# Kernel tuning notes

Hardware: AMD Instinct MI355X
Metric: run time of the kernel (lower is better)

## Reference

```python
import jax, jax.numpy as jnp
import numpy as np

N_NODES = 100000
N_EDGES = 3200000
D_IN = 128
D_OUT = 128
LN_EPS = 1e-5


def setup_inputs() -> dict:
    key = jax.random.key(0)
    k1, k2, k3, k4 = jax.random.split(key, 4)
    x = jax.random.normal(k1, (N_NODES, D_IN), dtype=jnp.float32)
    edge_index = jax.random.randint(k2, (2, N_EDGES), 0, N_NODES, dtype=jnp.int64)
    edge_weight = jax.random.uniform(k3, (N_EDGES,), dtype=jnp.float32)
    W = jax.random.normal(k4, (D_IN, D_OUT), dtype=jnp.float32) * (1.0 / np.sqrt(D_IN))
    b = jnp.zeros((D_OUT,), dtype=jnp.float32)
    gamma = jnp.ones((D_OUT,), dtype=jnp.float32)
    beta = jnp.zeros((D_OUT,), dtype=jnp.float32)
    return {"x": x, "edge_index": edge_index, "edge_weight": edge_weight,
            "W": W, "b": b, "gamma": gamma, "beta": beta}


def _gcn_layer(x, edge_index, edge_weight, W, b, gamma, beta):
    n = x.shape[0]
    row, col = edge_index[0], edge_index[1]  # source -> target
    # add self-loops with weight 1 (PyG GCNConv default)
    loop = jnp.arange(n, dtype=edge_index.dtype)
    row_f = jnp.concatenate([row, loop])
    col_f = jnp.concatenate([col, loop])
    w_f = jnp.concatenate([edge_weight, jnp.ones((n,), dtype=edge_weight.dtype)])
    # symmetric normalization: deg^-1/2[row] * w * deg^-1/2[col]
    deg = jax.ops.segment_sum(w_f, col_f, num_segments=n)
    dis = jnp.where(deg > 0, jax.lax.rsqrt(jnp.maximum(deg, 1e-30)), 0.0)
    norm = dis[row_f] * w_f * dis[col_f]  # [E+N]
    # linear transform first (cheaper), then gather/scatter-add over edges
    h = x @ W  # [N, D_OUT]
    msgs = norm[:, None] * h[row_f]  # [E+N, D_OUT]
    agg = jax.ops.segment_sum(msgs, col_f, num_segments=n) + b
    # LayerNorm over features
    mu = jnp.mean(agg, axis=-1, keepdims=True)
    var = jnp.mean(jnp.square(agg - mu), axis=-1, keepdims=True)
    normed = (agg - mu) * jax.lax.rsqrt(var + LN_EPS) * gamma + beta
    # ReLU; dropout is identity in eval mode
    return jax.nn.relu(normed)


def reference(x, edge_index, edge_weight, W, b, gamma, beta):
    return _gcn_layer(x, edge_index, edge_weight, W, b, gamma, beta)
```

## Files before the change

kernel.cpp:

```cpp
#include <hip/hip_runtime.h>

#define LN_EPS 1e-5f
#define FIX_SCALE 33554432.0f
#define FIX_INV   (1.0f / 33554432.0f)
#define MASK40    ((1ULL << 40) - 1)

__device__ __forceinline__ unsigned pack_bf16x2(float lo, float hi) {
    unsigned a = __float_as_uint(lo), b = __float_as_uint(hi);
    a = (a + 0x7FFFu + ((a >> 16) & 1u)) >> 16;
    b = (b + 0x7FFFu + ((b >> 16) & 1u)) >> 16;
    return a | (b << 16);
}

__device__ __forceinline__ float2 unpack_bf16x2(unsigned u) {
    return make_float2(__uint_as_float(u << 16), __uint_as_float(u & 0xFFFF0000u));
}


__global__ __launch_bounds__(256) void init_packed(unsigned long long* __restrict__ packed, int n) {
    int i = blockIdx.x * 256 + threadIdx.x;
    if (i < n) packed[i] = (1ULL << 25);
}


__global__ __launch_bounds__(256) void gemm_hist(const float* __restrict__ x,
                                                 const float* __restrict__ W,
                                                 unsigned* __restrict__ hb, int n,
                                                 const int* __restrict__ ei,
                                                 const float* __restrict__ ew,
                                                 unsigned long long* __restrict__ packed,
                                                 unsigned short* __restrict__ rank,
                                                 int E, int histBlocks) {
    __shared__ float xt[128][64];
    __shared__ float Ws[128][64];
    const int tid = threadIdx.x;

    if ((int)blockIdx.x < histBlocks) {
        int e = blockIdx.x * 256 + tid;
        if (e < E) {
            int c = ei[(long long)E + e];
            unsigned long long inc = (1ULL << 40) | (unsigned long long)(ew[e] * FIX_SCALE + 0.5f);
            unsigned long long old = atomicAdd(&packed[c], inc);
            rank[e] = (unsigned short)(old >> 40);
        }
        return;
    }

    const int g = (int)blockIdx.x - histBlocks;
    const int brow = (g >> 1) * 64;
    const int chalf = g & 1;

    for (int i = tid; i < 64 * 32; i += 256) {
        int r = i >> 5, c4 = i & 31, k0 = c4 * 4;
        int gr = brow + r;
        float4 v = make_float4(0.f, 0.f, 0.f, 0.f);
        if (gr < n) v = *(const float4*)(x + (size_t)gr * 128 + k0);
        xt[k0 + 0][r] = v.x; xt[k0 + 1][r] = v.y;
        xt[k0 + 2][r] = v.z; xt[k0 + 3][r] = v.w;
    }
    for (int i = tid; i < 128 * 16; i += 256) {
        int k = i >> 4, c4 = i & 15;
        float4 v = *(const float4*)(W + (size_t)k * 128 + chalf * 64 + c4 * 4);
        *(float4*)&Ws[k][c4 * 4] = v;
    }
    __syncthreads();

    const int r0 = (tid >> 4) * 4;
    const int c0 = (tid & 15) * 4;
    float4 acc0 = make_float4(0, 0, 0, 0), acc1 = acc0, acc2 = acc0, acc3 = acc0;
    #pragma unroll 8
    for (int k = 0; k < 128; k++) {
        float4 xa = *(const float4*)&xt[k][r0];
        float4 wb = *(const float4*)&Ws[k][c0];
        acc0.x += xa.x * wb.x; acc0.y += xa.x * wb.y; acc0.z += xa.x * wb.z; acc0.w += xa.x * wb.w;
        acc1.x += xa.y * wb.x; acc1.y += xa.y * wb.y; acc1.z += xa.y * wb.z; acc1.w += xa.y * wb.w;
        acc2.x += xa.z * wb.x; acc2.y += xa.z * wb.y; acc2.z += xa.z * wb.z; acc2.w += xa.z * wb.w;
        acc3.x += xa.w * wb.x; acc3.y += xa.w * wb.y; acc3.z += xa.w * wb.z; acc3.w += xa.w * wb.w;
    }
    float4 accs[4] = {acc0, acc1, acc2, acc3};
    #pragma unroll
    for (int i = 0; i < 4; i++) {
        int gr = brow + r0 + i;
        if (gr < n) {
            uint2 p;
            p.x = pack_bf16x2(accs[i].x, accs[i].y);
            p.y = pack_bf16x2(accs[i].z, accs[i].w);
            *(uint2*)(hb + (size_t)gr * 64 + (chalf * 64 + c0) / 2) = p;
        }
    }
}

__global__ __launch_bounds__(256) void hist_edges_plain(const int* __restrict__ ei,
                                                        const float* __restrict__ w,
                                                        unsigned long long* __restrict__ packed, int E) {
    int e = blockIdx.x * 256 + threadIdx.x;
    if (e >= E) return;
    int c = ei[(long long)E + e];
    unsigned long long inc = (1ULL << 40) | (unsigned long long)(w[e] * FIX_SCALE + 0.5f);
    atomicAdd(&packed[c], inc);
}

__global__ __launch_bounds__(256) void gemm_xw(const float* __restrict__ x,
                                               const float* __restrict__ W,
                                               unsigned* __restrict__ hb, int n) {
    __shared__ float xt[128][64];
    __shared__ float Ws[128][64];
    const int tid = threadIdx.x;
    const int brow = blockIdx.x * 64;
    const int chalf = blockIdx.y;

    for (int i = tid; i < 64 * 32; i += 256) {
        int r = i >> 5, c4 = i & 31, k0 = c4 * 4;
        int gr = brow + r;
        float4 v = make_float4(0.f, 0.f, 0.f, 0.f);
        if (gr < n) v = *(const float4*)(x + (size_t)gr * 128 + k0);
        xt[k0 + 0][r] = v.x; xt[k0 + 1][r] = v.y;
        xt[k0 + 2][r] = v.z; xt[k0 + 3][r] = v.w;
    }
    for (int i = tid; i < 128 * 16; i += 256) {
        int k = i >> 4, c4 = i & 15;
        float4 v = *(const float4*)(W + (size_t)k * 128 + chalf * 64 + c4 * 4);
        *(float4*)&Ws[k][c4 * 4] = v;
    }
    __syncthreads();

    const int r0 = (tid >> 4) * 4;
    const int c0 = (tid & 15) * 4;
    float4 acc0 = make_float4(0, 0, 0, 0), acc1 = acc0, acc2 = acc0, acc3 = acc0;
    #pragma unroll 8
    for (int k = 0; k < 128; k++) {
        float4 xa = *(const float4*)&xt[k][r0];
        float4 wb = *(const float4*)&Ws[k][c0];
        acc0.x += xa.x * wb.x; acc0.y += xa.x * wb.y; acc0.z += xa.x * wb.z; acc0.w += xa.x * wb.w;
        acc1.x += xa.y * wb.x; acc1.y += xa.y * wb.y; acc1.z += xa.y * wb.z; acc1.w += xa.y * wb.w;
        acc2.x += xa.z * wb.x; acc2.y += xa.z * wb.y; acc2.z += xa.z * wb.z; acc2.w += xa.z * wb.w;
        acc3.x += xa.w * wb.x; acc3.y += xa.w * wb.y; acc3.z += xa.w * wb.z; acc3.w += xa.w * wb.w;
    }
    float4 accs[4] = {acc0, acc1, acc2, acc3};
    #pragma unroll
    for (int i = 0; i < 4; i++) {
        int gr = brow + r0 + i;
        if (gr < n) {
            uint2 p;
            p.x = pack_bf16x2(accs[i].x, accs[i].y);
            p.y = pack_bf16x2(accs[i].z, accs[i].w);
            *(uint2*)(hb + (size_t)gr * 64 + (chalf * 64 + c0) / 2) = p;
        }
    }
}


__global__ __launch_bounds__(256) void scan_bsums_dis(const unsigned long long* __restrict__ packed,
                                                      int* __restrict__ bsum,
                                                      float* __restrict__ dis, int n) {
    int base = blockIdx.x * 1024;
    int t = threadIdx.x;
    int s = 0;
    #pragma unroll
    for (int k = 0; k < 4; k++) {
        int i = base + t * 4 + k;
        if (i < n) {
            unsigned long long p = packed[i];
            s += (int)(p >> 40);
            float d = (float)(p & MASK40) * FIX_INV;
            dis[i] = rsqrtf(fmaxf(d, 1e-30f));
        }
    }
    #pragma unroll
    for (int off = 32; off; off >>= 1) s += __shfl_xor(s, off);
    __shared__ int wsum[4];
    if ((t & 63) == 0) wsum[t >> 6] = s;
    __syncthreads();
    if (t == 0) bsum[blockIdx.x] = wsum[0] + wsum[1] + wsum[2] + wsum[3];
}

__global__ __launch_bounds__(256) void scan_boff(const int* __restrict__ bsum,
                                                 int* __restrict__ boff, int B,
                                                 int* __restrict__ rp, int n, int E) {
    int t = threadIdx.x;
    int v[4]; int loc = 0;
    #pragma unroll
    for (int k = 0; k < 4; k++) {
        int i = t * 4 + k;
        v[k] = (i < B) ? bsum[i] : 0;
        loc += v[k];
    }
    int lane = t & 63, wv = t >> 6;
    int incl = loc;
    #pragma unroll
    for (int off = 1; off < 64; off <<= 1) {
        int tt = __shfl_up(incl, off);
        if (lane >= off) incl += tt;
    }
    __shared__ int wsum[4];
    if (lane == 63) wsum[wv] = incl;
    __syncthreads();
    int woff = 0;
    for (int k = 0; k < wv; k++) woff += wsum[k];
    int run = woff + incl - loc;
    #pragma unroll
    for (int k = 0; k < 4; k++) {
        int i = t * 4 + k;
        if (i < B) boff[i] = run;
        run += v[k];
    }
    if (t == 0) rp[n] = E;
}

__global__ __launch_bounds__(256) void scan_write(const unsigned long long* __restrict__ packed,
                                                  const int* __restrict__ boff,
                                                  int* __restrict__ rp, int n) {
    int base = blockIdx.x * 1024;
    int t = threadIdx.x;
    int v[4]; int loc = 0;
    #pragma unroll
    for (int k = 0; k < 4; k++) {
        int i = base + t * 4 + k;
        v[k] = (i < n) ? (int)(packed[i] >> 40) : 0;
        loc += v[k];
    }
    int lane = t & 63, wv = t >> 6;
    int incl = loc;
    #pragma unroll
    for (int off = 1; off < 64; off <<= 1) {
        int tt = __shfl_up(incl, off);
        if (lane >= off) incl += tt;
    }
    __shared__ int wsum[4];
    if (lane == 63) wsum[wv] = incl;
    __syncthreads();
    int woff = 0;
    for (int k = 0; k < wv; k++) woff += wsum[k];
    int run = boff[blockIdx.x] + woff + incl - loc;
    #pragma unroll
    for (int k = 0; k < 4; k++) {
        int i = base + t * 4 + k;
        if (i < n) { rp[i] = run; run += v[k]; }
    }
}


__global__ __launch_bounds__(256) void sort_edges_rank(const int* __restrict__ ei,
                                                       const float* __restrict__ w,
                                                       const float* __restrict__ dis,
                                                       const int* __restrict__ rp,
                                                       const unsigned short* __restrict__ rank,
                                                       int2* __restrict__ es, int E) {
    int e = blockIdx.x * 256 + threadIdx.x;
    if (e >= E) return;
    int r = ei[e], c = ei[(long long)E + e];
    int pos = rp[c] + (int)rank[e];
    es[pos] = make_int2(r, __float_as_int(dis[r] * w[e]));
}

__global__ __launch_bounds__(256) void sort_edges_cursor(const int* __restrict__ ei,
                                                         const float* __restrict__ w,
                                                         const float* __restrict__ dis,
                                                         const int* __restrict__ rp,
                                                         int* __restrict__ cursor,
                                                         int2* __restrict__ es, int E) {
    int e = blockIdx.x * 256 + threadIdx.x;
    if (e >= E) return;
    int r = ei[e], c = ei[(long long)E + e];
    int pos = rp[c] + atomicAdd(&cursor[c], 1);
    es[pos] = make_int2(r, __float_as_int(dis[r] * w[e]));
}


__global__ __launch_bounds__(256) void agg_ln(const int* __restrict__ rp,
                                              const int2* __restrict__ es,
                                              const unsigned* __restrict__ hb,
                                              const float* __restrict__ dis,
                                              const float* __restrict__ b,
                                              const float* __restrict__ gamma,
                                              const float* __restrict__ beta,
                                              float* __restrict__ out, int n) {
    const int wave = threadIdx.x >> 6;
    const int lane = threadIdx.x & 63;
    const int node = blockIdx.x * 4 + wave;
    if (node >= n) return;

    const int j0 = rp[node], j1 = rp[node + 1];
    const float ds = dis[node];

    float2 hs = unpack_bf16x2(hb[(size_t)node * 64 + lane]);
    float ax = ds * hs.x, ay = ds * hs.y;

    int j = j0;
    for (; j + 7 < j1; j += 8) {
        int2 ee[8]; unsigned uu[8];
        #pragma unroll
        for (int k = 0; k < 8; k++) ee[k] = es[j + k];
        #pragma unroll
        for (int k = 0; k < 8; k++) uu[k] = hb[(size_t)ee[k].x * 64 + lane];
        #pragma unroll
        for (int k = 0; k < 8; k++) {
            float c = __int_as_float(ee[k].y);
            float2 v = unpack_bf16x2(uu[k]);
            ax += c * v.x;
            ay += c * v.y;
        }
    }
    for (; j < j1; ++j) {
        int2 e0 = es[j];
        float2 v = unpack_bf16x2(hb[(size_t)e0.x * 64 + lane]);
        float c = __int_as_float(e0.y);
        ax += c * v.x;
        ay += c * v.y;
    }

    float2 bb = ((const float2*)b)[lane];
    float vx = ds * ax + bb.x;
    float vy = ds * ay + bb.y;

    float s = vx + vy;
    #pragma unroll
    for (int off = 32; off; off >>= 1) s += __shfl_xor(s, off);
    float mu = s * (1.0f / 128.0f);
    float dx = vx - mu, dy = vy - mu;
    float q = dx * dx + dy * dy;
    #pragma unroll
    for (int off = 32; off; off >>= 1) q += __shfl_xor(q, off);
    float rs = rsqrtf(q * (1.0f / 128.0f) + LN_EPS);

    float2 g = ((const float2*)gamma)[lane], be = ((const float2*)beta)[lane];
    float2 o;
    o.x = fmaxf(dx * rs * g.x + be.x, 0.f);
    o.y = fmaxf(dy * rs * g.y + be.y, 0.f);
    ((float2*)(out + (size_t)node * 128))[lane] = o;
}


extern "C" void kernel_launch(void* const* d_in, const int* in_sizes, int n_in,
                              void* d_out, int out_size, void* d_ws, size_t ws_size,
                              hipStream_t stream) {
    const float* x     = (const float*)d_in[0];
    const int*   ei    = (const int*)d_in[1];
    const float* ew    = (const float*)d_in[2];
    const float* W     = (const float*)d_in[3];
    const float* b     = (const float*)d_in[4];
    const float* gamma = (const float*)d_in[5];
    const float* beta  = (const float*)d_in[6];

    const int n = in_sizes[0] / 128;
    const int E = in_sizes[2];
    float* out = (float*)d_out;

    char* ws = (char*)d_ws;
    const size_t MB = 1u << 20;

    unsigned long long* packed = (unsigned long long*)(ws);
    float* dis  = (float*)(ws + 1 * MB);
    int*   rp   = (int*)(ws + 1 * MB + 512 * 1024);
    int*   bsum = (int*)(ws + 2 * MB);
    int*   boff = (int*)(ws + 2 * MB + 64 * 1024);

    const int B = (n + 1023) / 1024;

    size_t esA_off = 10 * MB;
    size_t hA_off  = esA_off + (size_t)E * 8;
    size_t needA   = hA_off + (size_t)n * 128 * 2;
    size_t esB_off = 3 * MB;
    size_t hB_off  = esB_off + (size_t)E * 8;

    init_packed<<<(n + 255) / 256, 256, 0, stream>>>(packed, n);

    if (ws_size >= needA) {
        unsigned short* rank = (unsigned short*)(ws + 3 * MB);
        int2*     es = (int2*)(ws + esA_off);
        unsigned* hb = (unsigned*)(ws + hA_off);

        const int histBlocks = (E + 255) / 256;
        const int gemmBlocks = ((n + 63) / 64) * 2;
        gemm_hist<<<histBlocks + gemmBlocks, 256, 0, stream>>>(
            x, W, hb, n, ei, ew, packed, rank, E, histBlocks);

        scan_bsums_dis<<<B, 256, 0, stream>>>(packed, bsum, dis, n);
        scan_boff<<<1, 256, 0, stream>>>(bsum, boff, B, rp, n, E);
        scan_write<<<B, 256, 0, stream>>>(packed, boff, rp, n);
        sort_edges_rank<<<(E + 255) / 256, 256, 0, stream>>>(ei, ew, dis, rp, rank, es, E);

        agg_ln<<<(n + 3) / 4, 256, 0, stream>>>(rp, es, hb, dis, b, gamma, beta, out, n);
    } else {
        int*      cursor = (int*)(ws + 2 * MB + 256 * 1024);
        int2*     es = (int2*)(ws + esB_off);
        unsigned* hb = (unsigned*)(ws + hB_off);

        hipMemsetAsync(cursor, 0, (size_t)n * sizeof(int), stream);
        hist_edges_plain<<<(E + 255) / 256, 256, 0, stream>>>(ei, ew, packed, E);
        scan_bsums_dis<<<B, 256, 0, stream>>>(packed, bsum, dis, n);
        scan_boff<<<1, 256, 0, stream>>>(bsum, boff, B, rp, n, E);
        scan_write<<<B, 256, 0, stream>>>(packed, boff, rp, n);
        sort_edges_cursor<<<(E + 255) / 256, 256, 0, stream>>>(ei, ew, dis, rp, cursor, es, E);

        dim3 ggrid((n + 63) / 64, 2);
        gemm_xw<<<ggrid, 256, 0, stream>>>(x, W, hb, n);
        agg_ln<<<(n + 3) / 4, 256, 0, stream>>>(rp, es, hb, dis, b, gamma, beta, out, n);
    }
}
```

Before: 556.3 us.

## Shrink GEMM shared tiles via K-chunking and interleave GEMM blocks among histogram blocks

The fused GEMM+histogram kernel now stages x and W in 32-wide K chunks, so shared memory per block drops from 64KB to about 17KB, and launch bounds request 8 blocks per CU. The x tile is padded to 68 columns to reduce bank conflicts on the transposed writes. GEMM blocks are spread evenly across the grid instead of all following the histogram blocks, so the compute-bound GEMM overlaps the atomic-bound histogram work. In exchange there are extra barriers per K chunk and possible register pressure from the occupancy hint.

Measured after the change: 487.2 us. -12.4%, faster.

```diff
diff --git a/kernel.cpp b/kernel.cpp
--- a/kernel.cpp
+++ b/kernel.cpp
@@ -23,20 +23,24 @@
 }
 
 
-__global__ __launch_bounds__(256) void gemm_hist(const float* __restrict__ x,
-                                                 const float* __restrict__ W,
-                                                 unsigned* __restrict__ hb, int n,
-                                                 const int* __restrict__ ei,
-                                                 const float* __restrict__ ew,
-                                                 unsigned long long* __restrict__ packed,
-                                                 unsigned short* __restrict__ rank,
-                                                 int E, int histBlocks) {
-    __shared__ float xt[128][64];
-    __shared__ float Ws[128][64];
+__global__ __launch_bounds__(256, 8) void gemm_hist(const float* __restrict__ x,
+                                                    const float* __restrict__ W,
+                                                    unsigned* __restrict__ hb, int n,
+                                                    const int* __restrict__ ei,
+                                                    const float* __restrict__ ew,
+                                                    unsigned long long* __restrict__ packed,
+                                                    unsigned short* __restrict__ rank,
+                                                    int E, int G, int T) {
+    __shared__ float xt[32][68];
+    __shared__ float Ws[32][64];
     const int tid = threadIdx.x;
-
-    if ((int)blockIdx.x < histBlocks) {
-        int e = blockIdx.x * 256 + tid;
+    const int bid = (int)blockIdx.x;
+
+    const int g0 = (int)(((long long)bid * G) / T);
+    const int g1 = (int)(((long long)(bid + 1) * G) / T);
+
+    if (g1 == g0) {
+        int e = (bid - g0) * 256 + tid;
         if (e < E) {
             int c = ei[(long long)E + e];
             unsigned long long inc = (1ULL << 40) | (unsigned long long)(ew[e] * FIX_SCALE + 0.5f);
@@ -46,37 +50,46 @@
         return;
     }
 
-    const int g = (int)blockIdx.x - histBlocks;
+    const int g = g0;
     const int brow = (g >> 1) * 64;
     const int chalf = g & 1;
-
-    for (int i = tid; i < 64 * 32; i += 256) {
-        int r = i >> 5, c4 = i & 31, k0 = c4 * 4;
-        int gr = brow + r;
-        float4 v = make_float4(0.f, 0.f, 0.f, 0.f);
-        if (gr < n) v = *(const float4*)(x + (size_t)gr * 128 + k0);
-        xt[k0 + 0][r] = v.x; xt[k0 + 1][r] = v.y;
-        xt[k0 + 2][r] = v.z; xt[k0 + 3][r] = v.w;
-    }
-    for (int i = tid; i < 128 * 16; i += 256) {
-        int k = i >> 4, c4 = i & 15;
-        float4 v = *(const float4*)(W + (size_t)k * 128 + chalf * 64 + c4 * 4);
-        *(float4*)&Ws[k][c4 * 4] = v;
-    }
-    __syncthreads();
 
     const int r0 = (tid >> 4) * 4;
     const int c0 = (tid & 15) * 4;
     float4 acc0 = make_float4(0, 0, 0, 0), acc1 = acc0, acc2 = acc0, acc3 = acc0;
-    #pragma unroll 8
-    for (int k = 0; k < 128; k++) {
-        float4 xa = *(const float4*)&xt[k][r0];
-        float4 wb = *(const float4*)&Ws[k][c0];
-        acc0.x += xa.x * wb.x; acc0.y += xa.x * wb.y; acc0.z += xa.x * wb.z; acc0.w += xa.x * wb.w;
-        acc1.x += xa.y * wb.x; acc1.y += xa.y * wb.y; acc1.z += xa.y * wb.z; acc1.w += xa.y * wb.w;
-        acc2.x += xa.z * wb.x; acc2.y += xa.z * wb.y; acc2.z += xa.z * wb.z; acc2.w += xa.z * wb.w;
-        acc3.x += xa.w * wb.x; acc3.y += xa.w * wb.y; acc3.z += xa.w * wb.z; acc3.w += xa.w * wb.w;
-    }
+
+    for (int kc = 0; kc < 4; kc++) {
+        if (kc) __syncthreads();
+        #pragma unroll
+        for (int ii = 0; ii < 2; ii++) {
+            int i = tid + ii * 256;
+            int r = i >> 3, c4 = i & 7, kl = c4 * 4;
+            int gr = brow + r;
+            float4 v = make_float4(0.f, 0.f, 0.f, 0.f);
+            if (gr < n) v = *(const float4*)(x + (size_t)gr * 128 + kc * 32 + kl);
+            xt[kl + 0][r] = v.x; xt[kl + 1][r] = v.y;
+            xt[kl + 2][r] = v.z; xt[kl + 3][r] = v.w;
+        }
+        #pragma unroll
+        for (int ii = 0; ii < 2; ii++) {
+            int i = tid + ii * 256;
+            int k = i >> 4, c4 = i & 15;
+            float4 v = *(const float4*)(W + (size_t)(kc * 32 + k) * 128 + chalf * 64 + c4 * 4);
+            *(float4*)&Ws[k][c4 * 4] = v;
+        }
+        __syncthreads();
+
+        #pragma unroll 8
+        for (int k = 0; k < 32; k++) {
+            float4 xa = *(const float4*)&xt[k][r0];
+            float4 wb = *(const float4*)&Ws[k][c0];
+            acc0.x += xa.x * wb.x; acc0.y += xa.x * wb.y; acc0.z += xa.x * wb.z; acc0.w += xa.x * wb.w;
+            acc1.x += xa.y * wb.x; acc1.y += xa.y * wb.y; acc1.z += xa.y * wb.z; acc1.w += xa.y * wb.w;
+            acc2.x += xa.z * wb.x; acc2.y += xa.z * wb.y; acc2.z += xa.z * wb.z; acc2.w += xa.z * wb.w;
+            acc3.x += xa.w * wb.x; acc3.y += xa.w * wb.y; acc3.z += xa.w * wb.z; acc3.w += xa.w * wb.w;
+        }
+    }
+
     float4 accs[4] = {acc0, acc1, acc2, acc3};
     #pragma unroll
     for (int i = 0; i < 4; i++) {
@@ -372,8 +385,9 @@
 
         const int histBlocks = (E + 255) / 256;
         const int gemmBlocks = ((n + 63) / 64) * 2;
-        gemm_hist<<<histBlocks + gemmBlocks, 256, 0, stream>>>(
-            x, W, hb, n, ei, ew, packed, rank, E, histBlocks);
+        const int T = histBlocks + gemmBlocks;
+        gemm_hist<<<T, 256, 0, stream>>>(x, W, hb, n, ei, ew, packed, rank, E,
+                                         gemmBlocks, T);
 
         scan_bsums_dis<<<B, 256, 0, stream>>>(packed, bsum, dis, n);
         scan_boff<<<1, 256, 0, stream>>>(bsum, boff, B, rp, n, E);
```
